# Kernel tuning notes

Measured on AMD Instinct MI355X. Metric: run time of the kernel, lower is better.

The kernel has to match this reference:

```python
import jax, jax.numpy as jnp
import numpy as np

N_VERTS = 8192
N_FACES = 16384


def _safe_norm(d):
    # Euclidean length per row; zero-length edges get length 0 (matches sqrt(0))
    d2 = (d * d).sum(-1)
    return jnp.where(d2 > 0, jnp.sqrt(jnp.where(d2 > 0, d2, 1.0)), 0.0)


def _cotangent(V, F):
    # V: [N,3], F: [F,3] -> C: [F,3] cotangent weights for edges (23, 31, 12)
    v1 = V[F[:, 0]]
    v2 = V[F[:, 1]]
    v3 = V[F[:, 2]]
    l1 = _safe_norm(v2 - v3)
    l2 = _safe_norm(v3 - v1)
    l3 = _safe_norm(v1 - v2)
    sp = (l1 + l2 + l3) * 0.5
    s = sp * (sp - l1) * (sp - l2) * (sp - l3)
    # A = 2*sqrt(s); torch code replaces A<=0 or NaN by 1.0 -> s>0 captures both
    A = jnp.where(s > 0, 2.0 * jnp.sqrt(jnp.where(s > 0, s, 1.0)), 1.0)
    cot23 = l2 ** 2 + l3 ** 2 - l1 ** 2
    cot31 = l1 ** 2 + l3 ** 2 - l2 ** 2
    cot12 = l1 ** 2 + l2 ** 2 - l3 ** 2
    return jnp.stack([cot23, cot31, cot12], axis=1) / A[:, None] / 4.0


def setup_inputs() -> dict:
    key = jax.random.key(0)
    kv, kf = jax.random.split(key)
    V = jax.random.normal(kv, (N_VERTS, 3), dtype=jnp.float32)
    F = jax.random.randint(kf, (N_FACES, 3), 0, N_VERTS, dtype=jnp.int64)
    return {"V": V, "F": F}


def reference(V, F):
    # cot=True path of Laplacian.forward, batch size 1.
    N = V.shape[0]
    C = _cotangent(V, F)                      # [F,3]
    rows = F[:, jnp.array([1, 2, 0])].reshape(-1)  # edge opposite-vertex pairs
    cols = F[:, jnp.array([2, 0, 1])].reshape(-1)
    vals = C.reshape(-1)
    # sparse scatter-add into dense (scipy csr_matrix sums duplicates, as does .at[].add)
    W = jnp.zeros((N, N), dtype=V.dtype).at[rows, cols].add(vals)
    W = W + W.T
    L = jnp.diag(W.sum(axis=1)) - W           # M - L in the original
    return L
```

## Files before the change

### kernel.cpp

```cpp
#include <hip/hip_runtime.h>
#include <math.h>


__global__ void face_scatter_kernel(const float* __restrict__ V,
                                    const int* __restrict__ Fw,
                                    float* __restrict__ L,
                                    int nF, int N) {
    int f = blockIdx.x * blockDim.x + threadIdx.x;
    if (f >= nF) return;

    const bool is64 = (Fw[1] == 0) && (Fw[3] == 0) && (Fw[5] == 0) &&
                      (Fw[7] == 0) && (Fw[9] == 0) && (Fw[11] == 0);

    int i0, i1, i2;
    if (is64) {
        const int base = f * 6;
        i0 = Fw[base + 0];
        i1 = Fw[base + 2];
        i2 = Fw[base + 4];
    } else {
        const int base = f * 3;
        i0 = Fw[base + 0];
        i1 = Fw[base + 1];
        i2 = Fw[base + 2];
    }

    const float ax = V[i0 * 3 + 0], ay = V[i0 * 3 + 1], az = V[i0 * 3 + 2];
    const float bx = V[i1 * 3 + 0], by = V[i1 * 3 + 1], bz = V[i1 * 3 + 2];
    const float cx = V[i2 * 3 + 0], cy = V[i2 * 3 + 1], cz = V[i2 * 3 + 2];

    float dx, dy, dz, d2;
    dx = bx - cx; dy = by - cy; dz = bz - cz;
    d2 = dx * dx + dy * dy + dz * dz;
    const float l1 = (d2 > 0.0f) ? sqrtf(d2) : 0.0f;
    dx = cx - ax; dy = cy - ay; dz = cz - az;
    d2 = dx * dx + dy * dy + dz * dz;
    const float l2 = (d2 > 0.0f) ? sqrtf(d2) : 0.0f;
    dx = ax - bx; dy = ay - by; dz = az - bz;
    d2 = dx * dx + dy * dy + dz * dz;
    const float l3 = (d2 > 0.0f) ? sqrtf(d2) : 0.0f;

    const float sp = (l1 + l2 + l3) * 0.5f;
    const float s  = sp * (sp - l1) * (sp - l2) * (sp - l3);
    const float A  = (s > 0.0f) ? 2.0f * sqrtf(s) : 1.0f;

    const float c0 = ((l2 * l2 + l3 * l3 - l1 * l1) / A) * 0.25f;
    const float c1 = ((l1 * l1 + l3 * l3 - l2 * l2) / A) * 0.25f;
    const float c2 = ((l1 * l1 + l2 * l2 - l3 * l3) / A) * 0.25f;

    const size_t n = (size_t)N;
    {
        const int r = i1, c = i2; const float v = c0;
        atomicAdd(&L[(size_t)r * n + c], -v);
        atomicAdd(&L[(size_t)c * n + r], -v);
        atomicAdd(&L[(size_t)r * n + r],  v);
        atomicAdd(&L[(size_t)c * n + c],  v);
    }
    {
        const int r = i2, c = i0; const float v = c1;
        atomicAdd(&L[(size_t)r * n + c], -v);
        atomicAdd(&L[(size_t)c * n + r], -v);
        atomicAdd(&L[(size_t)r * n + r],  v);
        atomicAdd(&L[(size_t)c * n + c],  v);
    }
    {
        const int r = i0, c = i1; const float v = c2;
        atomicAdd(&L[(size_t)r * n + c], -v);
        atomicAdd(&L[(size_t)c * n + r], -v);
        atomicAdd(&L[(size_t)r * n + r],  v);
        atomicAdd(&L[(size_t)c * n + c],  v);
    }
}

extern "C" void kernel_launch(void* const* d_in, const int* in_sizes, int n_in,
                              void* d_out, int out_size, void* d_ws, size_t ws_size,
                              hipStream_t stream) {
    const float* V = (const float*)d_in[0];
    const int* Fw  = (const int*)d_in[1];
    float* L       = (float*)d_out;

    const int N  = in_sizes[0] / 3;
    const int nF = in_sizes[1] / 3;

    hipMemsetAsync(d_out, 0, (size_t)out_size * sizeof(float), stream);

    const int block = 256;
    const int grid = (nF + block - 1) / block;
    face_scatter_kernel<<<grid, block, 0, stream>>>(V, Fw, L, nF, N);
}
```

Baseline: 51.23 us.

## Bin edge contributions per row, then build dense rows in shared memory

Replaces the full-matrix memset followed by scattered global atomics with two phases. The first phase bins each off-diagonal contribution into a fixed-capacity per-row bucket and accumulates the diagonal separately. The second phase builds each dense row in shared memory and writes it out with vectorised stores, so the output is written exactly once and no separate memset of the 256MB matrix is needed. Rows with more than CAP entries would silently drop contributions, and the new path runs only when the workspace is large enough.

```diff
diff --git a/kernel.cpp b/kernel.cpp
--- a/kernel.cpp
+++ b/kernel.cpp
@@ -2,29 +2,22 @@
 #include <math.h>
 
 
-__global__ void face_scatter_kernel(const float* __restrict__ V,
-                                    const int* __restrict__ Fw,
-                                    float* __restrict__ L,
-                                    int nF, int N) {
-    int f = blockIdx.x * blockDim.x + threadIdx.x;
-    if (f >= nF) return;
+#define CAP 256
 
-    const bool is64 = (Fw[1] == 0) && (Fw[3] == 0) && (Fw[5] == 0) &&
-                      (Fw[7] == 0) && (Fw[9] == 0) && (Fw[11] == 0);
-
-    int i0, i1, i2;
+__device__ __forceinline__ void load_face(const int* __restrict__ Fw, int f, bool is64,
+                                          int& i0, int& i1, int& i2) {
     if (is64) {
         const int base = f * 6;
-        i0 = Fw[base + 0];
-        i1 = Fw[base + 2];
-        i2 = Fw[base + 4];
+        i0 = Fw[base + 0]; i1 = Fw[base + 2]; i2 = Fw[base + 4];
     } else {
         const int base = f * 3;
-        i0 = Fw[base + 0];
-        i1 = Fw[base + 1];
-        i2 = Fw[base + 2];
+        i0 = Fw[base + 0]; i1 = Fw[base + 1]; i2 = Fw[base + 2];
     }
+}
 
+__device__ __forceinline__ void cot_weights(const float* __restrict__ V,
+                                            int i0, int i1, int i2,
+                                            float& c0, float& c1, float& c2) {
     const float ax = V[i0 * 3 + 0], ay = V[i0 * 3 + 1], az = V[i0 * 3 + 2];
     const float bx = V[i1 * 3 + 0], by = V[i1 * 3 + 1], bz = V[i1 * 3 + 2];
     const float cx = V[i2 * 3 + 0], cy = V[i2 * 3 + 1], cz = V[i2 * 3 + 2];
@@ -44,27 +37,84 @@
     const float s  = sp * (sp - l1) * (sp - l2) * (sp - l3);
     const float A  = (s > 0.0f) ? 2.0f * sqrtf(s) : 1.0f;
 
-    const float c0 = ((l2 * l2 + l3 * l3 - l1 * l1) / A) * 0.25f;
-    const float c1 = ((l1 * l1 + l3 * l3 - l2 * l2) / A) * 0.25f;
-    const float c2 = ((l1 * l1 + l2 * l2 - l3 * l3) / A) * 0.25f;
+    c0 = ((l2 * l2 + l3 * l3 - l1 * l1) / A) * 0.25f;
+    c1 = ((l1 * l1 + l3 * l3 - l2 * l2) / A) * 0.25f;
+    c2 = ((l1 * l1 + l2 * l2 - l3 * l3) / A) * 0.25f;
+}
 
+__global__ void bin_faces_kernel(const float* __restrict__ V, const int* __restrict__ Fw,
+                                 int* __restrict__ cnt, float* __restrict__ diag,
+                                 int* __restrict__ cols, float* __restrict__ vals,
+                                 int nF) {
+    int f = blockIdx.x * blockDim.x + threadIdx.x;
+    if (f >= nF) return;
+
+    const bool is64 = (Fw[1] == 0) && (Fw[3] == 0) && (Fw[5] == 0) &&
+                      (Fw[7] == 0) && (Fw[9] == 0) && (Fw[11] == 0);
+
+    int i0, i1, i2;
+    load_face(Fw, f, is64, i0, i1, i2);
+    float c0, c1, c2;
+    cot_weights(V, i0, i1, i2, c0, c1, c2);
+
+    const int rr[3] = {i1, i2, i0};
+    const int cc[3] = {i2, i0, i1};
+    const float vv[3] = {c0, c1, c2};
+#pragma unroll
+    for (int t = 0; t < 3; ++t) {
+        const int r = rr[t], c = cc[t];
+        const float v = vv[t];
+        int idx = atomicAdd(&cnt[r], 1);
+        if (idx < CAP) { cols[(size_t)r * CAP + idx] = c; vals[(size_t)r * CAP + idx] = -v; }
+        idx = atomicAdd(&cnt[c], 1);
+        if (idx < CAP) { cols[(size_t)c * CAP + idx] = r; vals[(size_t)c * CAP + idx] = -v; }
+        atomicAdd(&diag[r], v);
+        atomicAdd(&diag[c], v);
+    }
+}
+
+__global__ void fill_rows_kernel(const int* __restrict__ cnt, const float* __restrict__ diag,
+                                 const int* __restrict__ cols, const float* __restrict__ vals,
+                                 float* __restrict__ L, int N) {
+    extern __shared__ float srow[];
+    const int row = blockIdx.x;
+    const int tid = threadIdx.x;
+    const int nv4 = N >> 2;
+
+    float4* s4 = (float4*)srow;
+    const float4 z = make_float4(0.f, 0.f, 0.f, 0.f);
+    for (int j = tid; j < nv4; j += blockDim.x) s4[j] = z;
+    __syncthreads();
+
+    int k = cnt[row];
+    if (k > CAP) k = CAP;
+    for (int t = tid; t < k; t += blockDim.x)
+        atomicAdd(&srow[cols[(size_t)row * CAP + t]], vals[(size_t)row * CAP + t]);
+    if (tid == 0) atomicAdd(&srow[row], diag[row]);
+    __syncthreads();
+
+    float4* out = (float4*)(L + (size_t)row * (size_t)N);
+    for (int j = tid; j < nv4; j += blockDim.x) out[j] = s4[j];
+}
+
+__global__ void face_scatter_kernel(const float* __restrict__ V, const int* __restrict__ Fw,
+                                    float* __restrict__ L, int nF, int N) {
+    int f = blockIdx.x * blockDim.x + threadIdx.x;
+    if (f >= nF) return;
+    const bool is64 = (Fw[1] == 0) && (Fw[3] == 0) && (Fw[5] == 0) &&
+                      (Fw[7] == 0) && (Fw[9] == 0) && (Fw[11] == 0);
+    int i0, i1, i2;
+    load_face(Fw, f, is64, i0, i1, i2);
+    float c0, c1, c2;
+    cot_weights(V, i0, i1, i2, c0, c1, c2);
+    const int rr[3] = {i1, i2, i0};
+    const int cc[3] = {i2, i0, i1};
+    const float vv[3] = {c0, c1, c2};
     const size_t n = (size_t)N;
-    {
-        const int r = i1, c = i2; const float v = c0;
-        atomicAdd(&L[(size_t)r * n + c], -v);
-        atomicAdd(&L[(size_t)c * n + r], -v);
-        atomicAdd(&L[(size_t)r * n + r],  v);
-        atomicAdd(&L[(size_t)c * n + c],  v);
-    }
-    {
-        const int r = i2, c = i0; const float v = c1;
-        atomicAdd(&L[(size_t)r * n + c], -v);
-        atomicAdd(&L[(size_t)c * n + r], -v);
-        atomicAdd(&L[(size_t)r * n + r],  v);
-        atomicAdd(&L[(size_t)c * n + c],  v);
-    }
-    {
-        const int r = i0, c = i1; const float v = c2;
+#pragma unroll
+    for (int t = 0; t < 3; ++t) {
+        const int r = rr[t], c = cc[t];
+        const float v = vv[t];
         atomicAdd(&L[(size_t)r * n + c], -v);
         atomicAdd(&L[(size_t)c * n + r], -v);
         atomicAdd(&L[(size_t)r * n + r],  v);
@@ -82,9 +132,26 @@
     const int N  = in_sizes[0] / 3;
     const int nF = in_sizes[1] / 3;
 
-    hipMemsetAsync(d_out, 0, (size_t)out_size * sizeof(float), stream);
+    const size_t need = (size_t)N * 4 + (size_t)N * 4 +
+                        (size_t)N * CAP * 4 + (size_t)N * CAP * 4;
 
-    const int block = 256;
-    const int grid = (nF + block - 1) / block;
-    face_scatter_kernel<<<grid, block, 0, stream>>>(V, Fw, L, nF, N);
+    if (ws_size >= need) {
+        int*   cnt  = (int*)d_ws;
+        float* diag = (float*)((char*)d_ws + (size_t)N * 4);
+        int*   cols = (int*)((char*)d_ws + (size_t)N * 8);
+        float* vals = (float*)((char*)d_ws + (size_t)N * 8 + (size_t)N * CAP * 4);
+
+        hipMemsetAsync(d_ws, 0, (size_t)N * 8, stream);
+
+        const int block = 256;
+        bin_faces_kernel<<<(nF + block - 1) / block, block, 0, stream>>>(
+            V, Fw, cnt, diag, cols, vals, nF);
+
+        fill_rows_kernel<<<N, block, (size_t)N * sizeof(float), stream>>>(
+            cnt, diag, cols, vals, L, N);
+    } else {
+        hipMemsetAsync(d_out, 0, (size_t)out_size * sizeof(float), stream);
+        const int block = 256;
+        face_scatter_kernel<<<(nF + block - 1) / block, block, 0, stream>>>(V, Fw, L, nF, N);
+    }
 }
```

Result: slower. 59.99 us (+17.1%).

## Fuse output zeroing and face scatter into one cooperative kernel with grid sync

Applied to the files above, without the earlier changes.

Replaces the separate memset plus scatter launch with a single cooperative kernel. It first zeroes the 256MB dense output using vectorized float4 stores across a fixed 1024x256 grid, then does a grid-wide sync and has a subset of threads per block run the face scatter with atomics. This removes one launch and the memset, at the cost of a grid barrier. Only 16 of 256 threads per block do scatter work, and the cooperative launch needs every block co-resident.

```diff
diff --git a/kernel.cpp b/kernel.cpp
--- a/kernel.cpp
+++ b/kernel.cpp
@@ -1,30 +1,18 @@
 #include <hip/hip_runtime.h>
+#include <hip/hip_cooperative_groups.h>
 #include <math.h>
 
+namespace cg = cooperative_groups;
 
-__global__ void face_scatter_kernel(const float* __restrict__ V,
-                                    const int* __restrict__ Fw,
-                                    float* __restrict__ L,
-                                    int nF, int N) {
-    int f = blockIdx.x * blockDim.x + threadIdx.x;
-    if (f >= nF) return;
 
-    const bool is64 = (Fw[1] == 0) && (Fw[3] == 0) && (Fw[5] == 0) &&
-                      (Fw[7] == 0) && (Fw[9] == 0) && (Fw[11] == 0);
+#define NB 1024
+#define NT 256
 
-    int i0, i1, i2;
-    if (is64) {
-        const int base = f * 6;
-        i0 = Fw[base + 0];
-        i1 = Fw[base + 2];
-        i2 = Fw[base + 4];
-    } else {
-        const int base = f * 3;
-        i0 = Fw[base + 0];
-        i1 = Fw[base + 1];
-        i2 = Fw[base + 2];
-    }
+typedef float v4f __attribute__((ext_vector_type(4)));
 
+__device__ __forceinline__ void cot_weights(const float* __restrict__ V,
+                                            int i0, int i1, int i2,
+                                            float& c0, float& c1, float& c2) {
     const float ax = V[i0 * 3 + 0], ay = V[i0 * 3 + 1], az = V[i0 * 3 + 2];
     const float bx = V[i1 * 3 + 0], by = V[i1 * 3 + 1], bz = V[i1 * 3 + 2];
     const float cx = V[i2 * 3 + 0], cy = V[i2 * 3 + 1], cz = V[i2 * 3 + 2];
@@ -44,32 +32,68 @@
     const float s  = sp * (sp - l1) * (sp - l2) * (sp - l3);
     const float A  = (s > 0.0f) ? 2.0f * sqrtf(s) : 1.0f;
 
-    const float c0 = ((l2 * l2 + l3 * l3 - l1 * l1) / A) * 0.25f;
-    const float c1 = ((l1 * l1 + l3 * l3 - l2 * l2) / A) * 0.25f;
-    const float c2 = ((l1 * l1 + l2 * l2 - l3 * l3) / A) * 0.25f;
+    c0 = ((l2 * l2 + l3 * l3 - l1 * l1) / A) * 0.25f;
+    c1 = ((l1 * l1 + l3 * l3 - l2 * l2) / A) * 0.25f;
+    c2 = ((l1 * l1 + l2 * l2 - l3 * l3) / A) * 0.25f;
+}
 
-    const size_t n = (size_t)N;
-    {
-        const int r = i1, c = i2; const float v = c0;
+__device__ __forceinline__ void scatter_face(const float* __restrict__ V,
+                                             const int* __restrict__ Fw,
+                                             float* __restrict__ L,
+                                             int f, bool is64, size_t n) {
+    int i0, i1, i2;
+    if (is64) { i0 = Fw[f * 6]; i1 = Fw[f * 6 + 2]; i2 = Fw[f * 6 + 4]; }
+    else      { i0 = Fw[f * 3]; i1 = Fw[f * 3 + 1]; i2 = Fw[f * 3 + 2]; }
+
+    float c0, c1, c2;
+    cot_weights(V, i0, i1, i2, c0, c1, c2);
+
+    const int rr_[3] = {i1, i2, i0};
+    const int cc_[3] = {i2, i0, i1};
+    const float vv_[3] = {c0, c1, c2};
+#pragma unroll
+    for (int t = 0; t < 3; ++t) {
+        const int r = rr_[t], c = cc_[t];
+        const float v = vv_[t];
         atomicAdd(&L[(size_t)r * n + c], -v);
         atomicAdd(&L[(size_t)c * n + r], -v);
         atomicAdd(&L[(size_t)r * n + r],  v);
         atomicAdd(&L[(size_t)c * n + c],  v);
     }
-    {
-        const int r = i2, c = i0; const float v = c1;
-        atomicAdd(&L[(size_t)r * n + c], -v);
-        atomicAdd(&L[(size_t)c * n + r], -v);
-        atomicAdd(&L[(size_t)r * n + r],  v);
-        atomicAdd(&L[(size_t)c * n + c],  v);
+}
+
+__global__ __launch_bounds__(NT, 4) void fused_zero_scatter_kernel(
+        const float* __restrict__ V, const int* __restrict__ Fw,
+        float* __restrict__ L, int nF, int N) {
+    const int tid = threadIdx.x;
+    const int bid = blockIdx.x;
+    const size_t gid = (size_t)bid * NT + tid;
+
+    const size_t total4 = ((size_t)N * (size_t)N) >> 2;
+    v4f* out4 = (v4f*)L;
+    for (size_t j = gid; j < total4; j += (size_t)NB * NT)
+        out4[j] = (v4f)0.0f;
+
+    cg::this_grid().sync();
+
+    const int fpb = (nF + NB - 1) / NB;
+    if (tid < fpb) {
+        const int f = bid * fpb + tid;
+        if (f < nF) {
+            const bool is64 = (Fw[1] == 0) && (Fw[3] == 0) && (Fw[5] == 0) &&
+                              (Fw[7] == 0) && (Fw[9] == 0) && (Fw[11] == 0);
+            scatter_face(V, Fw, L, f, is64, (size_t)N);
+        }
     }
-    {
-        const int r = i0, c = i1; const float v = c2;
-        atomicAdd(&L[(size_t)r * n + c], -v);
-        atomicAdd(&L[(size_t)c * n + r], -v);
-        atomicAdd(&L[(size_t)r * n + r],  v);
-        atomicAdd(&L[(size_t)c * n + c],  v);
-    }
+}
+
+__global__ void face_scatter_kernel(const float* __restrict__ V, const int* __restrict__ Fw,
+                                    float* __restrict__ L, int nF, int N) {
+    int f = blockIdx.x * blockDim.x + threadIdx.x;
+    if (f >= nF) return;
+    const bool is64 = (Fw[1] == 0) && (Fw[3] == 0) && (Fw[5] == 0) &&
+                      (Fw[7] == 0) && (Fw[9] == 0) && (Fw[11] == 0);
+    scatter_face(V, Fw, L, f, is64, (size_t)N);
 }
 
 extern "C" void kernel_launch(void* const* d_in, const int* in_sizes, int n_in,
@@ -79,12 +103,16 @@
     const int* Fw  = (const int*)d_in[1];
     float* L       = (float*)d_out;
 
-    const int N  = in_sizes[0] / 3;
-    const int nF = in_sizes[1] / 3;
+    int N  = in_sizes[0] / 3;
+    int nF = in_sizes[1] / 3;
 
-    hipMemsetAsync(d_out, 0, (size_t)out_size * sizeof(float), stream);
-
-    const int block = 256;
-    const int grid = (nF + block - 1) / block;
-    face_scatter_kernel<<<grid, block, 0, stream>>>(V, Fw, L, nF, N);
+    if ((N & 3) == 0 && (size_t)N * N >= (size_t)NB * NT * 4) {
+        void* args[] = {(void*)&V, (void*)&Fw, (void*)&L, (void*)&nF, (void*)&N};
+        hipLaunchCooperativeKernel((void*)fused_zero_scatter_kernel,
+                                   dim3(NB), dim3(NT), args, 0, stream);
+    } else {
+        hipMemsetAsync(d_out, 0, (size_t)out_size * sizeof(float), stream);
+        const int block = 256;
+        face_scatter_kernel<<<(nF + block - 1) / block, block, 0, stream>>>(V, Fw, L, nF, N);
+    }
 }
```

Result: slower. 197.3 us (+285.2%).
